# Performance work log

Hardware: AMD Instinct MI355X
Metric: run time of the kernel (lower is better)

The kernel has to match this reference:

```python
import jax, jax.numpy as jnp
import numpy as np


def setup_inputs() -> dict:
    key = jax.random.key(0)
    k1, k2 = jax.random.split(key)
    B, S, H = 32, 4096, 1024
    hidden = jax.random.normal(k1, (B, H), dtype=jnp.float32)
    encoder_outputs = jax.random.normal(k2, (B, S, H), dtype=jnp.float32)
    return {"hidden": hidden, "encoder_outputs": encoder_outputs}


def reference(hidden, encoder_outputs):
    # scores[b,s] = <encoder_outputs[b,s,:], hidden[b,:]>
    scores = jnp.einsum("bsh,bh->bs", encoder_outputs, hidden)  # [B,S]
    w = jax.nn.softmax(scores, axis=1)                           # [B,S]
    # context[b,h] = sum_s encoder_outputs[b,s,h] * w[b,s]
    context = jnp.einsum("bsh,bs->bh", encoder_outputs, w)      # [B,H]
    return context
```

## Files before the change

### kernel.cpp

```cpp
#include <hip/hip_runtime.h>
#include <math.h>

#define NB     32
#define WAVES  4
#define NTHR   256
#define HDIM   1024

__global__ __launch_bounds__(NTHR) void attn_pass1(
    const float* __restrict__ hidden,
    const float* __restrict__ enc,
    float* __restrict__ ws_c,
    float* __restrict__ ws_m,
    float* __restrict__ ws_l,
    int S)
{
    const int tid  = threadIdx.x;
    const int lane = tid & 63;
    const int w    = tid >> 6;
    const int b    = blockIdx.x / NB;
    const int blk  = blockIdx.x % NB;
    const int rowsPerBlock = S / NB;
    const int rowsPerWave  = rowsPerBlock / WAVES;
    const int s_base = blk * rowsPerBlock + w * rowsPerWave;

    const float4* h4 = reinterpret_cast<const float4*>(hidden + (size_t)b * HDIM);
    float4 hreg[4];
    #pragma unroll
    for (int q = 0; q < 4; ++q) hreg[q] = h4[q * 64 + lane];

    float c[16];
    #pragma unroll
    for (int k = 0; k < 16; ++k) c[k] = 0.f;
    float m = -INFINITY, lsum = 0.f;

    for (int i = 0; i < rowsPerWave; ++i) {
        const int s = s_base + i;
        const float4* row4 =
            reinterpret_cast<const float4*>(enc + ((size_t)b * S + s) * HDIM);
        float4 e[4];
        float part = 0.f;
        #pragma unroll
        for (int q = 0; q < 4; ++q) {
            e[q] = row4[q * 64 + lane];
            part += e[q].x * hreg[q].x + e[q].y * hreg[q].y
                  + e[q].z * hreg[q].z + e[q].w * hreg[q].w;
        }
        #pragma unroll
        for (int off = 32; off >= 1; off >>= 1)
            part += __shfl_xor(part, off);
        const float score = part;

        const float newm  = fmaxf(m, score);
        const float scale = __expf(m - newm);
        const float p     = __expf(score - newm);
        lsum = lsum * scale + p;
        const float* ef = reinterpret_cast<const float*>(e);
        #pragma unroll
        for (int k = 0; k < 16; ++k)
            c[k] = c[k] * scale + p * ef[k];
        m = newm;
    }

    __shared__ float lds_c[WAVES][HDIM];
    __shared__ float lds_m[WAVES];
    __shared__ float lds_l[WAVES];

    if (lane == 0) lds_m[w] = m;
    __syncthreads();
    const float M = fmaxf(fmaxf(lds_m[0], lds_m[1]), fmaxf(lds_m[2], lds_m[3]));
    const float f = __expf(m - M);
    if (lane == 0) lds_l[w] = lsum * f;
    #pragma unroll
    for (int q = 0; q < 4; ++q) {
        #pragma unroll
        for (int comp = 0; comp < 4; ++comp)
            lds_c[w][q * 256 + 4 * lane + comp] = c[q * 4 + comp] * f;
    }
    __syncthreads();

    const int pidx = b * NB + blk;
    float4 sum;
    {
        const int h = tid * 4;
        sum.x = lds_c[0][h+0] + lds_c[1][h+0] + lds_c[2][h+0] + lds_c[3][h+0];
        sum.y = lds_c[0][h+1] + lds_c[1][h+1] + lds_c[2][h+1] + lds_c[3][h+1];
        sum.z = lds_c[0][h+2] + lds_c[1][h+2] + lds_c[2][h+2] + lds_c[3][h+2];
        sum.w = lds_c[0][h+3] + lds_c[1][h+3] + lds_c[2][h+3] + lds_c[3][h+3];
    }
    reinterpret_cast<float4*>(ws_c)[(size_t)pidx * (HDIM / 4) + tid] = sum;
    if (tid == 0) {
        ws_m[pidx] = M;
        ws_l[pidx] = lds_l[0] + lds_l[1] + lds_l[2] + lds_l[3];
    }
}

__global__ __launch_bounds__(NTHR) void attn_pass2(
    const float* __restrict__ ws_c,
    const float* __restrict__ ws_m,
    const float* __restrict__ ws_l,
    float* __restrict__ out)
{
    const int b   = blockIdx.x;
    const int tid = threadIdx.x;

    float M = -INFINITY;
    #pragma unroll
    for (int j = 0; j < NB; ++j) M = fmaxf(M, ws_m[b * NB + j]);

    float L = 0.f;
    float4 acc = make_float4(0.f, 0.f, 0.f, 0.f);
    const float4* c4 = reinterpret_cast<const float4*>(ws_c);
    for (int j = 0; j < NB; ++j) {
        const float f = __expf(ws_m[b * NB + j] - M);
        L += ws_l[b * NB + j] * f;
        const float4 v = c4[(size_t)(b * NB + j) * (HDIM / 4) + tid];
        acc.x += v.x * f; acc.y += v.y * f; acc.z += v.z * f; acc.w += v.w * f;
    }
    const float inv = 1.f / L;
    float4 o = make_float4(acc.x * inv, acc.y * inv, acc.z * inv, acc.w * inv);
    reinterpret_cast<float4*>(out)[(size_t)b * (HDIM / 4) + tid] = o;
}

extern "C" void kernel_launch(void* const* d_in, const int* in_sizes, int n_in,
                              void* d_out, int out_size, void* d_ws, size_t ws_size,
                              hipStream_t stream) {
    const float* hidden = (const float*)d_in[0];
    const float* enc    = (const float*)d_in[1];
    float* out          = (float*)d_out;

    const int B = in_sizes[0] / HDIM;
    const int S = in_sizes[1] / in_sizes[0];

    float* ws_c = (float*)d_ws;
    float* ws_m = ws_c + (size_t)B * NB * HDIM;
    float* ws_l = ws_m + (size_t)B * NB;

    attn_pass1<<<B * NB, NTHR, 0, stream>>>(hidden, enc, ws_c, ws_m, ws_l, S);
    attn_pass2<<<B, NTHR, 0, stream>>>(ws_c, ws_m, ws_l, out);
}
```

Before: 109.1 us.

## Double-buffer encoder rows with nontemporal loads and two-row online softmax

Pass 1 now processes two rows per iteration and prefetches the next pair with nontemporal loads while computing the current pair, so more memory requests are in flight. The online softmax update is batched over both rows, and the rescale is skipped when the running max does not change. Launch bounds request higher occupancy. Pass 2 is split into 4x more 64-thread blocks to spread the final reduction across more CUs. The catches are higher register pressure from the double buffers, which the occupancy hint may force into spills, and a two-row loop that assumes an even rows-per-wave count.

```diff
diff --git a/kernel.cpp b/kernel.cpp
--- a/kernel.cpp
+++ b/kernel.cpp
@@ -6,7 +6,9 @@
 #define NTHR   256
 #define HDIM   1024
 
-__global__ __launch_bounds__(NTHR) void attn_pass1(
+typedef float floatv4 __attribute__((ext_vector_type(4)));
+
+__global__ __launch_bounds__(NTHR, 4) void attn_pass1(
     const float* __restrict__ hidden,
     const float* __restrict__ enc,
     float* __restrict__ ws_c,
@@ -23,8 +25,8 @@
     const int rowsPerWave  = rowsPerBlock / WAVES;
     const int s_base = blk * rowsPerBlock + w * rowsPerWave;
 
-    const float4* h4 = reinterpret_cast<const float4*>(hidden + (size_t)b * HDIM);
-    float4 hreg[4];
+    const floatv4* h4 = reinterpret_cast<const floatv4*>(hidden + (size_t)b * HDIM);
+    floatv4 hreg[4];
     #pragma unroll
     for (int q = 0; q < 4; ++q) hreg[q] = h4[q * 64 + lane];
 
@@ -33,32 +35,67 @@
     for (int k = 0; k < 16; ++k) c[k] = 0.f;
     float m = -INFINITY, lsum = 0.f;
 
-    for (int i = 0; i < rowsPerWave; ++i) {
-        const int s = s_base + i;
-        const float4* row4 =
-            reinterpret_cast<const float4*>(enc + ((size_t)b * S + s) * HDIM);
-        float4 e[4];
-        float part = 0.f;
+    const floatv4* row = reinterpret_cast<const floatv4*>(
+        enc + ((size_t)b * S + s_base) * HDIM) + lane;
+
+    floatv4 e0[4], e1[4];
+    #pragma unroll
+    for (int q = 0; q < 4; ++q) {
+        e0[q] = __builtin_nontemporal_load(&row[q * 64]);
+        e1[q] = __builtin_nontemporal_load(&row[256 + q * 64]);
+    }
+    row += 512;
+
+    for (int i = 0; i < rowsPerWave; i += 2) {
+        floatv4 f0[4], f1[4];
+        if (i + 2 < rowsPerWave) {
+            #pragma unroll
+            for (int q = 0; q < 4; ++q) {
+                f0[q] = __builtin_nontemporal_load(&row[q * 64]);
+                f1[q] = __builtin_nontemporal_load(&row[256 + q * 64]);
+            }
+            row += 512;
+        }
+
+        float p0 = 0.f, p1 = 0.f;
         #pragma unroll
         for (int q = 0; q < 4; ++q) {
-            e[q] = row4[q * 64 + lane];
-            part += e[q].x * hreg[q].x + e[q].y * hreg[q].y
-                  + e[q].z * hreg[q].z + e[q].w * hreg[q].w;
+            p0 += e0[q].x * hreg[q].x + e0[q].y * hreg[q].y
+                + e0[q].z * hreg[q].z + e0[q].w * hreg[q].w;
+            p1 += e1[q].x * hreg[q].x + e1[q].y * hreg[q].y
+                + e1[q].z * hreg[q].z + e1[q].w * hreg[q].w;
         }
         #pragma unroll
-        for (int off = 32; off >= 1; off >>= 1)
-            part += __shfl_xor(part, off);
-        const float score = part;
+        for (int off = 32; off >= 1; off >>= 1) {
+            p0 += __shfl_xor(p0, off);
+            p1 += __shfl_xor(p1, off);
+        }
+        const float s0 = p0, s1 = p1;
+        const float mx01 = fmaxf(s0, s1);
+        const float* e0f = reinterpret_cast<const float*>(e0);
+        const float* e1f = reinterpret_cast<const float*>(e1);
 
-        const float newm  = fmaxf(m, score);
-        const float scale = __expf(m - newm);
-        const float p     = __expf(score - newm);
-        lsum = lsum * scale + p;
-        const float* ef = reinterpret_cast<const float*>(e);
+        if (mx01 <= m) {
+            const float w0 = __expf(s0 - m);
+            const float w1 = __expf(s1 - m);
+            lsum += w0 + w1;
+            #pragma unroll
+            for (int k = 0; k < 16; ++k)
+                c[k] += w0 * e0f[k] + w1 * e1f[k];
+        } else {
+            const float newm  = mx01;
+            const float scale = __expf(m - newm);
+            const float w0 = __expf(s0 - newm);
+            const float w1 = __expf(s1 - newm);
+            lsum = lsum * scale + w0 + w1;
+            #pragma unroll
+            for (int k = 0; k < 16; ++k)
+                c[k] = c[k] * scale + w0 * e0f[k] + w1 * e1f[k];
+            m = newm;
+        }
+
         #pragma unroll
-        for (int k = 0; k < 16; ++k)
-            c[k] = c[k] * scale + p * ef[k];
-        m = newm;
+        for (int q = 0; q < 4; ++q) { e0[q] = f0[q]; e1[q] = f1[q]; }
     }
 
     __shared__ float lds_c[WAVES][HDIM];
@@ -94,14 +131,16 @@
     }
 }
 
-__global__ __launch_bounds__(NTHR) void attn_pass2(
+__global__ __launch_bounds__(64) void attn_pass2(
     const float* __restrict__ ws_c,
     const float* __restrict__ ws_m,
     const float* __restrict__ ws_l,
     float* __restrict__ out)
 {
-    const int b   = blockIdx.x;
-    const int tid = threadIdx.x;
+    const int b    = blockIdx.x >> 2;
+    const int quad = blockIdx.x & 3;
+    const int tid  = threadIdx.x;
+    const int v    = quad * 64 + tid;
 
     float M = -INFINITY;
     #pragma unroll
@@ -113,12 +152,12 @@
     for (int j = 0; j < NB; ++j) {
         const float f = __expf(ws_m[b * NB + j] - M);
         L += ws_l[b * NB + j] * f;
-        const float4 v = c4[(size_t)(b * NB + j) * (HDIM / 4) + tid];
-        acc.x += v.x * f; acc.y += v.y * f; acc.z += v.z * f; acc.w += v.w * f;
+        const float4 x = c4[(size_t)(b * NB + j) * (HDIM / 4) + v];
+        acc.x += x.x * f; acc.y += x.y * f; acc.z += x.z * f; acc.w += x.w * f;
     }
     const float inv = 1.f / L;
     float4 o = make_float4(acc.x * inv, acc.y * inv, acc.z * inv, acc.w * inv);
-    reinterpret_cast<float4*>(out)[(size_t)b * (HDIM / 4) + tid] = o;
+    reinterpret_cast<float4*>(out)[(size_t)b * (HDIM / 4) + v] = o;
 }
 
 extern "C" void kernel_launch(void* const* d_in, const int* in_sizes, int n_in,
@@ -136,5 +175,5 @@
     float* ws_l = ws_m + (size_t)B * NB;
 
     attn_pass1<<<B * NB, NTHR, 0, stream>>>(hidden, enc, ws_c, ws_m, ws_l, S);
-    attn_pass2<<<B, NTHR, 0, stream>>>(ws_c, ws_m, ws_l, out);
+    attn_pass2<<<B * 4, 64, 0, stream>>>(ws_c, ws_m, ws_l, out);
 }
```

Result: faster. 95.84 us (median of 2 runs) (-12.2%).
